# Performance work log

Measured on AMD Instinct MI355X. Metric: run time of the kernel, lower is better.

## Reference

```python
import jax, jax.numpy as jnp
import numpy as np

NUM_FEATURES = 64
# upper-triangular (i<j) index pairs in the same row-major order as the
# original nested loop: i outer, j inner with j > i
_IU, _JU = np.triu_indices(NUM_FEATURES, k=1)


def setup_inputs() -> dict:
    key = jax.random.key(0)
    x = jax.random.normal(key, (4096, NUM_FEATURES, 128), dtype=jnp.float32)
    return {"x": x}


def reference(x) -> jnp.ndarray:
    # Gram matrix of feature vectors: [B, F, F]
    gram = jnp.einsum("bfd,bgd->bfg", x, x)
    # gather strictly-upper-triangular entries -> [B, F*(F-1)/2]
    return gram[:, _IU, _JU]
```

## Files before the change

### kernel.cpp

```cpp
#include <hip/hip_runtime.h>

typedef __attribute__((ext_vector_type(4))) float f32x4;
typedef __attribute__((ext_vector_type(8))) short bf16x8;

constexpr int F = 64;
constexpr int D = 128;
constexpr int NPAIR = 2016;

__device__ inline unsigned short f2bf(float f) {
  unsigned int u = __float_as_uint(f);
  return (unsigned short)((u + 0x7FFFu + ((u >> 16) & 1u)) >> 16);
}

__global__ __launch_bounds__(256)
void gram_upper_kernel(const float* __restrict__ x, float* __restrict__ out) {
  __shared__ __align__(16) unsigned char lds[F * 256];

  const int b = blockIdx.x;
  const int t = threadIdx.x;
  const float* xb = x + (size_t)b * (F * D);

#pragma unroll
  for (int k = 0; k < 8; ++k) {
    int idx4 = t + 256 * k;
    f32x4 v = reinterpret_cast<const f32x4*>(xb)[idx4];
    int e  = idx4 << 2;
    int f  = e >> 7;
    int d0 = e & 127;
    int g  = d0 >> 3;
    int gs = g ^ (f & 15);
    unsigned int lo = (unsigned)f2bf(v.x) | ((unsigned)f2bf(v.y) << 16);
    unsigned int hi = (unsigned)f2bf(v.z) | ((unsigned)f2bf(v.w) << 16);
    uint2 pk; pk.x = lo; pk.y = hi;
    *reinterpret_cast<uint2*>(lds + f * 256 + gs * 16 + ((d0 & 7) ? 8 : 0)) = pk;
  }
  __syncthreads();

  const int w  = t >> 6;
  const int l  = t & 63;
  const int lr = l & 15;
  const int lk = l >> 4;

  f32x4 acc[4] = {f32x4{0,0,0,0}, f32x4{0,0,0,0}, f32x4{0,0,0,0}, f32x4{0,0,0,0}};

  const int rowA = w * 16 + lr;
#pragma unroll
  for (int kk = 0; kk < 4; ++kk) {
    int gl  = (kk << 2) + lk;
    int gsw = gl ^ lr;
    bf16x8 a = *reinterpret_cast<const bf16x8*>(lds + rowA * 256 + gsw * 16);
#pragma unroll
    for (int tj = 0; tj < 4; ++tj) {
      bf16x8 bb = *reinterpret_cast<const bf16x8*>(lds + (tj * 16 + lr) * 256 + gsw * 16);
      acc[tj] = __builtin_amdgcn_mfma_f32_16x16x32_bf16(a, bb, acc[tj], 0, 0, 0);
    }
  }

  float* ob = out + (size_t)b * NPAIR;
  const int ibase = w * 16 + lk * 4;
#pragma unroll
  for (int tj = 0; tj < 4; ++tj) {
    int j = tj * 16 + lr;
#pragma unroll
    for (int r = 0; r < 4; ++r) {
      int i = ibase + r;
      if (j > i) {
        int p = i * 63 - ((i * (i - 1)) >> 1) + (j - i - 1);
        ob[p] = acc[tj][r];
      }
    }
  }
}

extern "C" void kernel_launch(void* const* d_in, const int* in_sizes, int n_in,
                              void* d_out, int out_size, void* d_ws, size_t ws_size,
                              hipStream_t stream) {
  const float* x = (const float*)d_in[0];
  float* out = (float*)d_out;
  const int B = in_sizes[0] / (F * D);
  gram_upper_kernel<<<dim3(B), dim3(256), 0, stream>>>(x, out);
}
```

Before: 30.11 us.

## Process four batches per block with register prefetch and triangular-only tile compute

Each block now handles four batch items, loading the next batch's fp32 data into registers while the current one is computed from LDS (software double buffering). MFMA work is limited to the ten upper-triangular 16x16 tiles, balanced across the four waves, instead of all sixteen tiles. The intent is to hide global-load latency behind compute and drop redundant lower-triangle MFMAs. The cost is a smaller grid with fewer blocks, plus higher register pressure from the two 8-vector prefetch buffers.

```diff
diff --git a/kernel.cpp b/kernel.cpp
--- a/kernel.cpp
+++ b/kernel.cpp
@@ -6,69 +6,111 @@
 constexpr int F = 64;
 constexpr int D = 128;
 constexpr int NPAIR = 2016;
+constexpr int NB = 4;
 
-__device__ inline unsigned short f2bf(float f) {
-  unsigned int u = __float_as_uint(f);
-  return (unsigned short)((u + 0x7FFFu + ((u >> 16) & 1u)) >> 16);
+__device__ inline unsigned f2bf(float f) {
+  unsigned u = __float_as_uint(f);
+  return (u + 0x7FFFu + ((u >> 16) & 1u)) >> 16;
 }
 
-__global__ __launch_bounds__(256)
-void gram_upper_kernel(const float* __restrict__ x, float* __restrict__ out) {
+#define BAR() do { asm volatile("s_waitcnt lgkmcnt(0)" ::: "memory"); \
+                   __builtin_amdgcn_s_barrier(); \
+                   asm volatile("" ::: "memory"); } while (0)
+
+__global__ __launch_bounds__(256, 4)
+void gram_upper_kernel(const float* __restrict__ x, float* __restrict__ out,
+                       int Btot) {
   __shared__ __align__(16) unsigned char lds[F * 256];
 
-  const int b = blockIdx.x;
-  const int t = threadIdx.x;
-  const float* xb = x + (size_t)b * (F * D);
-
-#pragma unroll
-  for (int k = 0; k < 8; ++k) {
-    int idx4 = t + 256 * k;
-    f32x4 v = reinterpret_cast<const f32x4*>(xb)[idx4];
-    int e  = idx4 << 2;
-    int f  = e >> 7;
-    int d0 = e & 127;
-    int g  = d0 >> 3;
-    int gs = g ^ (f & 15);
-    unsigned int lo = (unsigned)f2bf(v.x) | ((unsigned)f2bf(v.y) << 16);
-    unsigned int hi = (unsigned)f2bf(v.z) | ((unsigned)f2bf(v.w) << 16);
-    uint2 pk; pk.x = lo; pk.y = hi;
-    *reinterpret_cast<uint2*>(lds + f * 256 + gs * 16 + ((d0 & 7) ? 8 : 0)) = pk;
-  }
-  __syncthreads();
-
+  const int t  = threadIdx.x;
   const int w  = t >> 6;
   const int l  = t & 63;
   const int lr = l & 15;
   const int lk = l >> 4;
 
-  f32x4 acc[4] = {f32x4{0,0,0,0}, f32x4{0,0,0,0}, f32x4{0,0,0,0}, f32x4{0,0,0,0}};
+  const long b0 = (long)blockIdx.x * NB;
 
-  const int rowA = w * 16 + lr;
+  f32x4 ra[8], rb[8];
+
+  auto loadb = [&](f32x4 (&r)[8], long batch) {
+    const f32x4* p = reinterpret_cast<const f32x4*>(x + batch * (F * D));
 #pragma unroll
-  for (int kk = 0; kk < 4; ++kk) {
-    int gl  = (kk << 2) + lk;
-    int gsw = gl ^ lr;
-    bf16x8 a = *reinterpret_cast<const bf16x8*>(lds + rowA * 256 + gsw * 16);
+    for (int k = 0; k < 8; ++k) r[k] = p[t + 256 * k];
+  };
+
+  auto stage = [&](const f32x4 (&r)[8]) {
 #pragma unroll
-    for (int tj = 0; tj < 4; ++tj) {
-      bf16x8 bb = *reinterpret_cast<const bf16x8*>(lds + (tj * 16 + lr) * 256 + gsw * 16);
-      acc[tj] = __builtin_amdgcn_mfma_f32_16x16x32_bf16(a, bb, acc[tj], 0, 0, 0);
+    for (int k = 0; k < 8; ++k) {
+      int idx4 = t + 256 * k;
+      int e    = idx4 << 2;
+      int f    = e >> 7;
+      int d0   = e & 127;
+      int off  = f * 256 + (((d0 >> 3) ^ (f & 15)) << 4) + ((d0 & 4) << 1);
+      uint2 pk;
+      pk.x = f2bf(r[k].x) | (f2bf(r[k].y) << 16);
+      pk.y = f2bf(r[k].z) | (f2bf(r[k].w) << 16);
+      *reinterpret_cast<uint2*>(lds + off) = pk;
     }
-  }
+  };
 
-  float* ob = out + (size_t)b * NPAIR;
-  const int ibase = w * 16 + lk * 4;
+  auto compute = [&](long batch) {
+    float* ob = out + batch * NPAIR;
+    unsigned desc = (w == 0) ? 0x03020100u : (w == 1) ? 0x03121103u
+                  : (w == 2) ? 0x02002213u : 0x02003323u;
+    int cnt = desc >> 24;
 #pragma unroll
-  for (int tj = 0; tj < 4; ++tj) {
-    int j = tj * 16 + lr;
+    for (int s = 0; s < 3; ++s) {
+      if (s < cnt) {
+        int ti = (desc >> (8 * s + 4)) & 15;
+        int tj = (desc >> (8 * s)) & 15;
+        f32x4 acc = {0.f, 0.f, 0.f, 0.f};
 #pragma unroll
-    for (int r = 0; r < 4; ++r) {
-      int i = ibase + r;
-      if (j > i) {
-        int p = i * 63 - ((i * (i - 1)) >> 1) + (j - i - 1);
-        ob[p] = acc[tj][r];
+        for (int kk = 0; kk < 4; ++kk) {
+          int gsw = ((kk << 2) + lk) ^ lr;
+          bf16x8 a  = *reinterpret_cast<const bf16x8*>(lds + (ti * 16 + lr) * 256 + gsw * 16);
+          bf16x8 bv = *reinterpret_cast<const bf16x8*>(lds + (tj * 16 + lr) * 256 + gsw * 16);
+          acc = __builtin_amdgcn_mfma_f32_16x16x32_bf16(a, bv, acc, 0, 0, 0);
+        }
+        int j  = tj * 16 + lr;
+        int ib = ti * 16 + lk * 4;
+#pragma unroll
+        for (int r = 0; r < 4; ++r) {
+          int i = ib + r;
+          if (j > i) {
+            int p = i * 63 - ((i * (i - 1)) >> 1) + (j - i - 1);
+            ob[p] = acc[r];
+          }
+        }
       }
     }
+  };
+
+  const bool v1 = (b0 + 1 < Btot), v2 = (b0 + 2 < Btot), v3 = (b0 + 3 < Btot);
+
+  loadb(ra, b0);
+  stage(ra);
+  if (v1) loadb(rb, b0 + 1);
+  BAR();
+  compute(b0);
+  BAR();
+  if (v1) {
+    stage(rb);
+    if (v2) loadb(ra, b0 + 2);
+    BAR();
+    compute(b0 + 1);
+    BAR();
+  }
+  if (v2) {
+    stage(ra);
+    if (v3) loadb(rb, b0 + 3);
+    BAR();
+    compute(b0 + 2);
+    BAR();
+  }
+  if (v3) {
+    stage(rb);
+    BAR();
+    compute(b0 + 3);
   }
 }
 
@@ -78,5 +120,6 @@
   const float* x = (const float*)d_in[0];
   float* out = (float*)d_out;
   const int B = in_sizes[0] / (F * D);
-  gram_upper_kernel<<<dim3(B), dim3(256), 0, stream>>>(x, out);
+  const int grid = (B + NB - 1) / NB;
+  gram_upper_kernel<<<dim3(grid), dim3(256), 0, stream>>>(x, out, B);
 }
```

New measurement: 31.70 us. +5.3%, slower.
